# Optimization experiments

Measured on AMD Instinct MI355X. Metric: run time of the kernel, lower is better.

## Reference

```python
import jax, jax.numpy as jnp
import numpy as np

N_NODES = 100000


def _gcn_layer(x, W, b, src, dst, n):
    # PyG GCNConv with default add_self_loops=True, symmetric normalization.
    h = x @ W  # [N, out]
    deg = jax.ops.segment_sum(jnp.ones_like(dst, dtype=h.dtype), dst, num_segments=n)
    dinv = jnp.where(deg > 0, jax.lax.rsqrt(deg), 0.0)
    norm = dinv[src] * dinv[dst]  # [E]
    msg = h[src] * norm[:, None]  # gather + scale
    out = jax.ops.segment_sum(msg, dst, num_segments=n)  # scatter-add at targets
    return out + b


def setup_inputs() -> dict:
    key = jax.random.key(0)
    ks = jax.random.split(key, 8)
    n, e = N_NODES, 3200000
    x = jax.random.normal(ks[0], (n, 16), dtype=jnp.float32)
    edge_index = jax.random.randint(ks[1], (2, e), 0, n, dtype=jnp.int64)
    def glorot(k, fi, fo):
        lim = float(np.sqrt(6.0 / (fi + fo)))
        return jax.random.uniform(k, (fi, fo), jnp.float32, -lim, lim)
    return {
        "x": x,
        "edge_index": edge_index,
        "W1": glorot(ks[2], 16, 32), "b1": jnp.zeros((32,), jnp.float32),
        "W2": glorot(ks[3], 32, 64), "b2": jnp.zeros((64,), jnp.float32),
        "W3": glorot(ks[4], 64, 1),  "b3": jnp.zeros((1,), jnp.float32),
    }


def reference(x, edge_index, W1, b1, W2, b2, W3, b3):
    n = x.shape[0]
    # add self-loops once (shared by all layers)
    loops = jnp.arange(n, dtype=edge_index.dtype)
    src = jnp.concatenate([edge_index[0], loops])
    dst = jnp.concatenate([edge_index[1], loops])
    h = _gcn_layer(x, W1, b1, src, dst, n)
    h = jax.nn.relu(h)  # dropout is identity in eval mode
    h = _gcn_layer(h, W2, b2, src, dst, n)
    h = jax.nn.relu(h)
    h = _gcn_layer(h, W3, b3, src, dst, n)
    return jax.nn.sigmoid(h)
```

## Files before the change

### kernel.cpp

```cpp
#include <hip/hip_runtime.h>
#include <hip/hip_bf16.h>
#include <math.h>


#define CW    128
#define CSH   7
#define MAXBUK 1024
#define EPB   8192
#define CAP   5120

static inline int cdiv(int a, int b) { return (a + b - 1) / b; }

__device__ inline unsigned int bf16_rn(float f) {
    unsigned int u = __float_as_uint(f);
    return (u + 0x7fffu + ((u >> 16) & 1u)) >> 16;
}
#define BLO(u) __uint_as_float((u) << 16)
#define BHI(u) __uint_as_float((u) & 0xffff0000u)

#define UNPACK_ADD(A, V) \
    A[0] += BLO(V.x); A[1] += BHI(V.x); \
    A[2] += BLO(V.y); A[3] += BHI(V.y); \
    A[4] += BLO(V.z); A[5] += BHI(V.z); \
    A[6] += BLO(V.w); A[7] += BHI(V.w);
#define UNPACK_ADD2(A, V) \
    A[0] += BLO(V.x); A[1] += BHI(V.x); \
    A[2] += BLO(V.y); A[3] += BHI(V.y);


__global__ void __launch_bounds__(256) k_bscatter(const int* __restrict__ src,
                                                  const int* __restrict__ dst,
                                                  int* __restrict__ gcur,
                                                  int* __restrict__ ebuf, int e, int nbuk) {
    __shared__ int lh[MAXBUK];
    __shared__ int lo[MAXBUK];
    __shared__ int lb[MAXBUK];
    __shared__ int sh[256];
    __shared__ int stage[EPB];
    __shared__ unsigned short bkOf[EPB];
    int4 db[8];
    int t = threadIdx.x;
    for (int b = t; b < nbuk; b += 256) lh[b] = 0;
    __syncthreads();
    int base4 = blockIdx.x * (EPB / 4);
    int e4 = e >> 2;
#pragma unroll
    for (int j = 0; j < 8; j++) {
        int i4 = base4 + j * 256 + t;
        if (i4 < e4) {
            int4 d = ((const int4*)dst)[i4];
            db[j] = d;
            atomicAdd(&lh[d.x >> CSH], 1); atomicAdd(&lh[d.y >> CSH], 1);
            atomicAdd(&lh[d.z >> CSH], 1); atomicAdd(&lh[d.w >> CSH], 1);
        } else db[j] = make_int4(-1, -1, -1, -1);
    }
    __syncthreads();
    int carry = 0;
    for (int cb = 0; cb < nbuk; cb += 256) {
        int b = cb + t;
        int c = (b < nbuk) ? lh[b] : 0;
        if (b < nbuk && c) lb[b] = b * CAP + atomicAdd(&gcur[b], c);
        sh[t] = c;
        __syncthreads();
        for (int o = 1; o < 256; o <<= 1) {
            int u = (t >= o) ? sh[t - o] : 0;
            __syncthreads();
            sh[t] += u;
            __syncthreads();
        }
        if (b < nbuk) lo[b] = sh[t] - c + carry;
        carry += sh[255];
        __syncthreads();
    }
    for (int b = t; b < nbuk; b += 256) lh[b] = 0;
    __syncthreads();
#pragma unroll
    for (int j = 0; j < 8; j++) {
        int i4 = base4 + j * 256 + t;
        if (i4 < e4) {
            int4 s = ((const int4*)src)[i4];
            int4 d = db[j];
            int dd, ss, b, r, slot;
#define PUT(DX, SX) \
            dd = DX; ss = SX; b = dd >> CSH; \
            r = atomicAdd(&lh[b], 1); slot = lo[b] + r; \
            stage[slot] = ((dd & (CW - 1)) << 17) | ss; \
            bkOf[slot] = (unsigned short)b;
            PUT(d.x, s.x) PUT(d.y, s.y) PUT(d.z, s.z) PUT(d.w, s.w)
#undef PUT
        }
    }
    __syncthreads();
    int tot = min(EPB, e - blockIdx.x * EPB);
#pragma unroll
    for (int j = 0; j < 32; j++) {
        int slot = j * 256 + t;
        if (slot < tot) {
            int b = bkOf[slot];
            ebuf[lb[b] + (slot - lo[b])] = stage[slot];
        }
    }
}


__global__ void __launch_bounds__(512) k_csr2(const int* __restrict__ ebuf,
                                              const int* __restrict__ gcur,
                                              int* __restrict__ rowstart,
                                              int* __restrict__ csr_src,
                                              float* __restrict__ dinv,
                                              const float* __restrict__ x,
                                              unsigned int* __restrict__ xs,
                                              int n, int e, int nbuk) {
    __shared__ int cnt[CW];
    __shared__ int offs[CW];
    __shared__ int red[512];
    int t = threadIdx.x;
    int bid = blockIdx.x;
    int part = 0;
    for (int j = t; j < bid; j += 512) part += gcur[j];
    red[t] = part;
    __syncthreads();
    for (int o = 256; o > 0; o >>= 1) {
        if (t < o) red[t] += red[t + o];
        __syncthreads();
    }
    int dbeg = red[0];
    if (t < CW) cnt[t] = 0;
    __syncthreads();
    int cnt_b = gcur[bid];
    const int4* eb4 = (const int4*)(ebuf + (size_t)bid * CAP);
    int n4 = (cnt_b + 3) >> 2;
    for (int k4 = t; k4 < n4; k4 += 512) {
        int4 v = eb4[k4];
        int rem = cnt_b - (k4 << 2);
        atomicAdd(&cnt[v.x >> 17], 1);
        if (rem > 1) atomicAdd(&cnt[v.y >> 17], 1);
        if (rem > 2) atomicAdd(&cnt[v.z >> 17], 1);
        if (rem > 3) atomicAdd(&cnt[v.w >> 17], 1);
    }
    __syncthreads();
    int v = (t < CW) ? cnt[t] : 0;
    if (t < CW) offs[t] = v;
    __syncthreads();
    for (int o = 1; o < CW; o <<= 1) {
        int u = (t < CW && t >= o) ? offs[t - o] : 0;
        __syncthreads();
        if (t < CW) offs[t] += u;
        __syncthreads();
    }
    int node = bid * CW + t;
    if (t < CW) {
        int ex = offs[t] - v;
        float dd = rsqrtf((float)v + 1.0f);
        if (node < n) {
            rowstart[node] = dbeg + ex;
            dinv[node] = dd;
            const float4* xr = (const float4*)(x + (size_t)node * 16);
            float4 v0 = xr[0], v1 = xr[1], v2 = xr[2], v3 = xr[3];
            uint4 o0, o1;
            o0.x = bf16_rn(v0.x * dd) | (bf16_rn(v0.y * dd) << 16);
            o0.y = bf16_rn(v0.z * dd) | (bf16_rn(v0.w * dd) << 16);
            o0.z = bf16_rn(v1.x * dd) | (bf16_rn(v1.y * dd) << 16);
            o0.w = bf16_rn(v1.z * dd) | (bf16_rn(v1.w * dd) << 16);
            o1.x = bf16_rn(v2.x * dd) | (bf16_rn(v2.y * dd) << 16);
            o1.y = bf16_rn(v2.z * dd) | (bf16_rn(v2.w * dd) << 16);
            o1.z = bf16_rn(v3.x * dd) | (bf16_rn(v3.y * dd) << 16);
            o1.w = bf16_rn(v3.z * dd) | (bf16_rn(v3.w * dd) << 16);
            uint4* xo = (uint4*)(xs + (size_t)node * 8);
            xo[0] = o0; xo[1] = o1;
        }
        cnt[t] = ex;
    }
    __syncthreads();
    for (int k4 = t; k4 < n4; k4 += 512) {
        int4 vv = eb4[k4];
        int rem = cnt_b - (k4 << 2);
        int pv, r;
#define SCAT(PV) pv = PV; r = atomicAdd(&cnt[pv >> 17], 1); csr_src[dbeg + r] = pv & 0x1FFFF;
        SCAT(vv.x)
        if (rem > 1) { SCAT(vv.y) }
        if (rem > 2) { SCAT(vv.z) }
        if (rem > 3) { SCAT(vv.w) }
#undef SCAT
    }
    if (bid == 0 && t == 0) rowstart[n] = e;
}


__global__ void __launch_bounds__(256) k_pull16(const int* __restrict__ rowstart,
                                                const int* __restrict__ csr_src,
                                                const float* __restrict__ dinv,
                                                const unsigned int* __restrict__ xs,
                                                float* __restrict__ agg16, int n) {
    int wid = (blockIdx.x * blockDim.x + threadIdx.x) >> 6;
    if (wid >= n) return;
    int lane = threadIdx.x & 63;
    int q = lane & 3;
    int beg = rowstart[wid], end = rowstart[wid + 1];
    const uint2* x2 = (const uint2*)xs;
    float dd = dinv[wid];
    uint2 sv = x2[(size_t)wid * 4 + q];
    float a0[4], a1[4];
#pragma unroll
    for (int i = 0; i < 4; i++) { a0[i] = 0.f; a1[i] = 0.f; }
    int k = beg + (lane >> 2);
    for (; k + 16 < end; k += 32) {
        int s0 = __builtin_nontemporal_load(csr_src + k);
        int s1 = __builtin_nontemporal_load(csr_src + k + 16);
        uint2 v0 = x2[(size_t)s0 * 4 + q];
        uint2 v1 = x2[(size_t)s1 * 4 + q];
        UNPACK_ADD2(a0, v0);
        UNPACK_ADD2(a1, v1);
    }
    if (k < end) {
        int s0 = __builtin_nontemporal_load(csr_src + k);
        uint2 v0 = x2[(size_t)s0 * 4 + q];
        UNPACK_ADD2(a0, v0);
    }
#pragma unroll
    for (int i = 0; i < 4; i++) a0[i] += a1[i];
#pragma unroll
    for (int off = 4; off < 64; off <<= 1)
#pragma unroll
        for (int i = 0; i < 4; i++) a0[i] += __shfl_xor(a0[i], off);
    UNPACK_ADD2(a0, sv);
    if (lane < 4)
        ((float4*)(agg16 + (size_t)wid * 16))[q] =
            make_float4(a0[0] * dd, a0[1] * dd, a0[2] * dd, a0[3] * dd);
}


__global__ void __launch_bounds__(256) k_dense1(const float* __restrict__ agg,
                                                const float* __restrict__ dinv,
                                                const float* __restrict__ W1,
                                                const float* __restrict__ b1,
                                                unsigned int* __restrict__ h1s, int n) {
    int node = blockIdx.x * 256 + threadIdx.x;
    if (node >= n) return;
    float dd = dinv[node];
    float in[16];
    const float4* a4 = (const float4*)(agg + (size_t)node * 16);
#pragma unroll
    for (int f = 0; f < 4; f++) {
        float4 v = a4[f];
        in[4 * f] = v.x; in[4 * f + 1] = v.y; in[4 * f + 2] = v.z; in[4 * f + 3] = v.w;
    }
    unsigned int hw[16];
#pragma unroll
    for (int c = 0; c < 16; c++) {
        float o0 = b1[2 * c], o1 = b1[2 * c + 1];
#pragma unroll
        for (int k = 0; k < 16; k++) {
            o0 += in[k] * W1[k * 32 + 2 * c];
            o1 += in[k] * W1[k * 32 + 2 * c + 1];
        }
        hw[c] = bf16_rn(fmaxf(o0, 0.f) * dd) | (bf16_rn(fmaxf(o1, 0.f) * dd) << 16);
    }
    uint4* o4 = (uint4*)(h1s + (size_t)node * 16);
    o4[0] = make_uint4(hw[0], hw[1], hw[2], hw[3]);
    o4[1] = make_uint4(hw[4], hw[5], hw[6], hw[7]);
    o4[2] = make_uint4(hw[8], hw[9], hw[10], hw[11]);
    o4[3] = make_uint4(hw[12], hw[13], hw[14], hw[15]);
}


__global__ void __launch_bounds__(256) k_pull32(const int* __restrict__ rowstart,
                                                const int* __restrict__ csr_src,
                                                const float* __restrict__ dinv,
                                                const unsigned int* __restrict__ h1s,
                                                float* __restrict__ agg32, int n) {
    int wid = (blockIdx.x * blockDim.x + threadIdx.x) >> 6;
    if (wid >= n) return;
    int lane = threadIdx.x & 63;
    int f4 = lane & 3;
    int beg = rowstart[wid], end = rowstart[wid + 1];
    const uint4* h4 = (const uint4*)h1s;
    float dd = dinv[wid];
    uint4 sv = h4[(size_t)wid * 4 + f4];
    float acc[8], ac1[8];
#pragma unroll
    for (int i = 0; i < 8; i++) { acc[i] = 0.f; ac1[i] = 0.f; }
    int k = beg + (lane >> 2);
    for (; k + 16 < end; k += 32) {
        int s0 = __builtin_nontemporal_load(csr_src + k);
        int s1 = __builtin_nontemporal_load(csr_src + k + 16);
        uint4 v0 = h4[(size_t)s0 * 4 + f4];
        uint4 v1 = h4[(size_t)s1 * 4 + f4];
        UNPACK_ADD(acc, v0);
        UNPACK_ADD(ac1, v1);
    }
    if (k < end) {
        int s0 = __builtin_nontemporal_load(csr_src + k);
        uint4 v0 = h4[(size_t)s0 * 4 + f4];
        UNPACK_ADD(acc, v0);
    }
#pragma unroll
    for (int i = 0; i < 8; i++) acc[i] += ac1[i];
#pragma unroll
    for (int off = 4; off < 64; off <<= 1)
#pragma unroll
        for (int i = 0; i < 8; i++) acc[i] += __shfl_xor(acc[i], off);
    UNPACK_ADD(acc, sv);
    if (lane < 4) {
        float4* o4 = (float4*)(agg32 + (size_t)wid * 32 + f4 * 8);
        o4[0] = make_float4(acc[0] * dd, acc[1] * dd, acc[2] * dd, acc[3] * dd);
        o4[1] = make_float4(acc[4] * dd, acc[5] * dd, acc[6] * dd, acc[7] * dd);
    }
}


__global__ void __launch_bounds__(256) k_dense2(const float* __restrict__ agg,
                                                const float* __restrict__ dinv,
                                                const float* __restrict__ W2,
                                                const float* __restrict__ b2,
                                                const float* __restrict__ W3,
                                                float* __restrict__ t2, int n) {
    int node = blockIdx.x * 256 + threadIdx.x;
    if (node >= n) return;
    float in[32];
    const float4* a4 = (const float4*)(agg + (size_t)node * 32);
#pragma unroll
    for (int f = 0; f < 8; f++) {
        float4 v = a4[f];
        in[4 * f] = v.x; in[4 * f + 1] = v.y; in[4 * f + 2] = v.z; in[4 * f + 3] = v.w;
    }
    float p = 0.f;
#pragma unroll
    for (int cb = 0; cb < 4; cb++) {
        float o[16];
#pragma unroll
        for (int c = 0; c < 16; c++) o[c] = b2[cb * 16 + c];
#pragma unroll
        for (int k = 0; k < 32; k++) {
            float ik = in[k];
#pragma unroll
            for (int c = 0; c < 16; c++) o[c] += ik * W2[k * 64 + cb * 16 + c];
        }
#pragma unroll
        for (int c = 0; c < 16; c++) p += fmaxf(o[c], 0.f) * W3[cb * 16 + c];
    }
    t2[node] = p * dinv[node];
}


__global__ void __launch_bounds__(256) k_pull1_sig(const int* __restrict__ rowstart,
                                                   const int* __restrict__ csr_src,
                                                   const float* __restrict__ dinv,
                                                   const float* __restrict__ t2,
                                                   const float* __restrict__ b3,
                                                   float* __restrict__ out, int n) {
    int tid = blockIdx.x * blockDim.x + threadIdx.x;
    int wid = tid >> 5;
    if (wid >= n) return;
    int lane32 = threadIdx.x & 31;
    int beg = rowstart[wid], end = rowstart[wid + 1];
    float selfv = t2[wid];
    float dd = dinv[wid];
    float acc = 0.f;
    for (int k = beg + lane32; k < end; k += 32)
        acc += t2[__builtin_nontemporal_load(csr_src + k)];
#pragma unroll
    for (int off = 1; off < 32; off <<= 1) acc += __shfl_xor(acc, off);
    if (lane32 == 0) {
        float v = (acc + selfv) * dd + b3[0];
        out[wid] = 1.0f / (1.0f + expf(-v));
    }
}


extern "C" void kernel_launch(void* const* d_in, const int* in_sizes, int n_in,
                              void* d_out, int out_size, void* d_ws, size_t ws_size,
                              hipStream_t stream) {
    const float* x  = (const float*)d_in[0];
    const int*   ei = (const int*)d_in[1];
    const float* W1 = (const float*)d_in[2];
    const float* b1 = (const float*)d_in[3];
    const float* W2 = (const float*)d_in[4];
    const float* b2 = (const float*)d_in[5];
    const float* W3 = (const float*)d_in[6];
    const float* b3 = (const float*)d_in[7];

    const int n = in_sizes[0] / 16;
    const int e = in_sizes[1] / 2;
    const int* src = ei;
    const int* dst = ei + e;
    const int nbuk = cdiv(n, CW);

    auto rup = [](size_t v) { return (v + 15) & ~(size_t)15; };
    char* wp = (char*)d_ws;
    auto alloc = [&](size_t elems) { void* p = wp; wp += rup(elems) * 4; return p; };
    int*   gcur     = (int*)  alloc(MAXBUK);
    float* dinv     = (float*)alloc(n);
    int*   rowstart = (int*)  alloc(n + 1);
    int*   ebuf     = (int*)  alloc((size_t)nbuk * CAP);
    int*   csr_src  = (int*)  alloc(e);
    unsigned int* xs  = (unsigned int*)alloc((size_t)8 * n);
    unsigned int* h1s = (unsigned int*)alloc((size_t)16 * n);
    float* agg16    = (float*)alloc((size_t)16 * n);
    float* agg32    = (float*)alloc((size_t)32 * n);
    float* t2       = (float*)alloc(n);

    float* out = (float*)d_out;
    const int B = 256;
    const int pullGrid = cdiv(n * 64, B);

    hipMemsetAsync(gcur, 0, MAXBUK * 4, stream);
    k_bscatter<<<cdiv(e, EPB), B, 0, stream>>>(src, dst, gcur, ebuf, e, nbuk);
    k_csr2<<<nbuk, 512, 0, stream>>>(ebuf, gcur, rowstart, csr_src,
                                     dinv, x, xs, n, e, nbuk);

    k_pull16<<<pullGrid, B, 0, stream>>>(rowstart, csr_src, dinv, xs, agg16, n);
    k_dense1<<<cdiv(n, B), B, 0, stream>>>(agg16, dinv, W1, b1, h1s, n);

    k_pull32<<<pullGrid, B, 0, stream>>>(rowstart, csr_src, dinv, h1s, agg32, n);
    k_dense2<<<cdiv(n, B), B, 0, stream>>>(agg32, dinv, W2, b2, W3, t2, n);

    k_pull1_sig<<<cdiv(n * 32, B), B, 0, stream>>>(rowstart, csr_src, dinv, t2, b3, out, n);
}
```

Baseline: 215.7 us.

## Fuse layer-1 pull with dense transform and deepen gather unrolling

Merges the first-layer neighbor aggregation and the 16→32 dense transform into one kernel. Partial aggregates are staged in shared memory and applied to W1 by 64 threads per block, which removes the agg16 round-trip and one launch. The gather loops in the pull kernels are unrolled to three independent accumulators, and the final pull to two, to keep more loads in flight. The cost is an added block-wide barrier and a dense phase that uses only a quarter of each block's threads, with strided per-thread stores to h1s.

```diff
diff --git a/kernel.cpp b/kernel.cpp
--- a/kernel.cpp
+++ b/kernel.cpp
@@ -187,80 +187,76 @@
 }
 
 
-__global__ void __launch_bounds__(256) k_pull16(const int* __restrict__ rowstart,
-                                                const int* __restrict__ csr_src,
-                                                const float* __restrict__ dinv,
-                                                const unsigned int* __restrict__ xs,
-                                                float* __restrict__ agg16, int n) {
-    int wid = (blockIdx.x * blockDim.x + threadIdx.x) >> 6;
-    if (wid >= n) return;
-    int lane = threadIdx.x & 63;
-    int q = lane & 3;
-    int beg = rowstart[wid], end = rowstart[wid + 1];
-    const uint2* x2 = (const uint2*)xs;
-    float dd = dinv[wid];
-    uint2 sv = x2[(size_t)wid * 4 + q];
-    float a0[4], a1[4];
-#pragma unroll
-    for (int i = 0; i < 4; i++) { a0[i] = 0.f; a1[i] = 0.f; }
-    int k = beg + (lane >> 2);
-    for (; k + 16 < end; k += 32) {
-        int s0 = __builtin_nontemporal_load(csr_src + k);
-        int s1 = __builtin_nontemporal_load(csr_src + k + 16);
-        uint2 v0 = x2[(size_t)s0 * 4 + q];
-        uint2 v1 = x2[(size_t)s1 * 4 + q];
-        UNPACK_ADD2(a0, v0);
-        UNPACK_ADD2(a1, v1);
-    }
-    if (k < end) {
-        int s0 = __builtin_nontemporal_load(csr_src + k);
-        uint2 v0 = x2[(size_t)s0 * 4 + q];
-        UNPACK_ADD2(a0, v0);
-    }
-#pragma unroll
-    for (int i = 0; i < 4; i++) a0[i] += a1[i];
-#pragma unroll
-    for (int off = 4; off < 64; off <<= 1)
-#pragma unroll
-        for (int i = 0; i < 4; i++) a0[i] += __shfl_xor(a0[i], off);
-    UNPACK_ADD2(a0, sv);
-    if (lane < 4)
-        ((float4*)(agg16 + (size_t)wid * 16))[q] =
-            make_float4(a0[0] * dd, a0[1] * dd, a0[2] * dd, a0[3] * dd);
-}
-
-
-__global__ void __launch_bounds__(256) k_dense1(const float* __restrict__ agg,
-                                                const float* __restrict__ dinv,
-                                                const float* __restrict__ W1,
-                                                const float* __restrict__ b1,
-                                                unsigned int* __restrict__ h1s, int n) {
-    int node = blockIdx.x * 256 + threadIdx.x;
-    if (node >= n) return;
-    float dd = dinv[node];
-    float in[16];
-    const float4* a4 = (const float4*)(agg + (size_t)node * 16);
-#pragma unroll
-    for (int f = 0; f < 4; f++) {
-        float4 v = a4[f];
-        in[4 * f] = v.x; in[4 * f + 1] = v.y; in[4 * f + 2] = v.z; in[4 * f + 3] = v.w;
-    }
-    unsigned int hw[16];
-#pragma unroll
-    for (int c = 0; c < 16; c++) {
-        float o0 = b1[2 * c], o1 = b1[2 * c + 1];
-#pragma unroll
-        for (int k = 0; k < 16; k++) {
-            o0 += in[k] * W1[k * 32 + 2 * c];
-            o1 += in[k] * W1[k * 32 + 2 * c + 1];
-        }
-        hw[c] = bf16_rn(fmaxf(o0, 0.f) * dd) | (bf16_rn(fmaxf(o1, 0.f) * dd) << 16);
-    }
-    uint4* o4 = (uint4*)(h1s + (size_t)node * 16);
-    o4[0] = make_uint4(hw[0], hw[1], hw[2], hw[3]);
-    o4[1] = make_uint4(hw[4], hw[5], hw[6], hw[7]);
-    o4[2] = make_uint4(hw[8], hw[9], hw[10], hw[11]);
-    o4[3] = make_uint4(hw[12], hw[13], hw[14], hw[15]);
+__global__ void __launch_bounds__(256) k_pull16d(const int* __restrict__ rowstart,
+                                                 const int* __restrict__ csr_src,
+                                                 const float* __restrict__ dinv,
+                                                 const unsigned int* __restrict__ xs,
+                                                 const float* __restrict__ W1,
+                                                 const float* __restrict__ b1,
+                                                 unsigned int* __restrict__ h1s, int n) {
+    __shared__ float sAgg[4][16];
+    __shared__ float sDd[4];
+    int t = threadIdx.x;
+    int wv = t >> 6;
+    int lane = t & 63;
+    int wid = blockIdx.x * 4 + wv;
+    if (wid < n) {
+        int q = lane & 3;
+        int beg = rowstart[wid], end = rowstart[wid + 1];
+        const uint2* x2 = (const uint2*)xs;
+        float dd = dinv[wid];
+        uint2 sv = x2[(size_t)wid * 4 + q];
+        float a0[4], a1[4], a2[4];
+#pragma unroll
+        for (int i = 0; i < 4; i++) { a0[i] = 0.f; a1[i] = 0.f; a2[i] = 0.f; }
+        int k = beg + (lane >> 2);
+        for (; k + 32 < end; k += 48) {
+            int s0 = __builtin_nontemporal_load(csr_src + k);
+            int s1 = __builtin_nontemporal_load(csr_src + k + 16);
+            int s2 = __builtin_nontemporal_load(csr_src + k + 32);
+            uint2 v0 = x2[(size_t)s0 * 4 + q];
+            uint2 v1 = x2[(size_t)s1 * 4 + q];
+            uint2 v2 = x2[(size_t)s2 * 4 + q];
+            UNPACK_ADD2(a0, v0);
+            UNPACK_ADD2(a1, v1);
+            UNPACK_ADD2(a2, v2);
+        }
+        for (; k < end; k += 16) {
+            int s0 = __builtin_nontemporal_load(csr_src + k);
+            uint2 v0 = x2[(size_t)s0 * 4 + q];
+            UNPACK_ADD2(a0, v0);
+        }
+#pragma unroll
+        for (int i = 0; i < 4; i++) a0[i] += a1[i] + a2[i];
+#pragma unroll
+        for (int off = 4; off < 64; off <<= 1)
+#pragma unroll
+            for (int i = 0; i < 4; i++) a0[i] += __shfl_xor(a0[i], off);
+        UNPACK_ADD2(a0, sv);
+        if (lane < 4) {
+#pragma unroll
+            for (int i = 0; i < 4; i++) sAgg[wv][q * 4 + i] = a0[i] * dd;
+            if (q == 0) sDd[wv] = dd;
+        }
+    }
+    __syncthreads();
+    if (t < 64) {
+        int w2 = t >> 4, c = t & 15;
+        int node = blockIdx.x * 4 + w2;
+        if (node < n) {
+            float dd = sDd[w2];
+            const float* a = sAgg[w2];
+            float o0 = b1[2 * c], o1 = b1[2 * c + 1];
+#pragma unroll
+            for (int k = 0; k < 16; k++) {
+                float av = a[k];
+                o0 += av * W1[k * 32 + 2 * c];
+                o1 += av * W1[k * 32 + 2 * c + 1];
+            }
+            h1s[(size_t)node * 16 + c] =
+                bf16_rn(fmaxf(o0, 0.f) * dd) | (bf16_rn(fmaxf(o1, 0.f) * dd) << 16);
+        }
+    }
 }
 
 
@@ -277,25 +273,28 @@
     const uint4* h4 = (const uint4*)h1s;
     float dd = dinv[wid];
     uint4 sv = h4[(size_t)wid * 4 + f4];
-    float acc[8], ac1[8];
-#pragma unroll
-    for (int i = 0; i < 8; i++) { acc[i] = 0.f; ac1[i] = 0.f; }
+    float acc[8], ac1[8], ac2[8];
+#pragma unroll
+    for (int i = 0; i < 8; i++) { acc[i] = 0.f; ac1[i] = 0.f; ac2[i] = 0.f; }
     int k = beg + (lane >> 2);
-    for (; k + 16 < end; k += 32) {
+    for (; k + 32 < end; k += 48) {
         int s0 = __builtin_nontemporal_load(csr_src + k);
         int s1 = __builtin_nontemporal_load(csr_src + k + 16);
+        int s2 = __builtin_nontemporal_load(csr_src + k + 32);
         uint4 v0 = h4[(size_t)s0 * 4 + f4];
         uint4 v1 = h4[(size_t)s1 * 4 + f4];
+        uint4 v2 = h4[(size_t)s2 * 4 + f4];
         UNPACK_ADD(acc, v0);
         UNPACK_ADD(ac1, v1);
-    }
-    if (k < end) {
+        UNPACK_ADD(ac2, v2);
+    }
+    for (; k < end; k += 16) {
         int s0 = __builtin_nontemporal_load(csr_src + k);
         uint4 v0 = h4[(size_t)s0 * 4 + f4];
         UNPACK_ADD(acc, v0);
     }
 #pragma unroll
-    for (int i = 0; i < 8; i++) acc[i] += ac1[i];
+    for (int i = 0; i < 8; i++) acc[i] += ac1[i] + ac2[i];
 #pragma unroll
     for (int off = 4; off < 64; off <<= 1)
 #pragma unroll
@@ -356,9 +355,14 @@
     int beg = rowstart[wid], end = rowstart[wid + 1];
     float selfv = t2[wid];
     float dd = dinv[wid];
-    float acc = 0.f;
-    for (int k = beg + lane32; k < end; k += 32)
+    float acc = 0.f, ac1 = 0.f;
+    int k = beg + lane32;
+    for (; k + 32 < end; k += 64) {
         acc += t2[__builtin_nontemporal_load(csr_src + k)];
+        ac1 += t2[__builtin_nontemporal_load(csr_src + k + 32)];
+    }
+    if (k < end) acc += t2[__builtin_nontemporal_load(csr_src + k)];
+    acc += ac1;
 #pragma unroll
     for (int off = 1; off < 32; off <<= 1) acc += __shfl_xor(acc, off);
     if (lane32 == 0) {
@@ -396,23 +400,20 @@
     int*   csr_src  = (int*)  alloc(e);
     unsigned int* xs  = (unsigned int*)alloc((size_t)8 * n);
     unsigned int* h1s = (unsigned int*)alloc((size_t)16 * n);
-    float* agg16    = (float*)alloc((size_t)16 * n);
     float* agg32    = (float*)alloc((size_t)32 * n);
     float* t2       = (float*)alloc(n);
 
     float* out = (float*)d_out;
     const int B = 256;
-    const int pullGrid = cdiv(n * 64, B);
 
     hipMemsetAsync(gcur, 0, MAXBUK * 4, stream);
     k_bscatter<<<cdiv(e, EPB), B, 0, stream>>>(src, dst, gcur, ebuf, e, nbuk);
     k_csr2<<<nbuk, 512, 0, stream>>>(ebuf, gcur, rowstart, csr_src,
                                      dinv, x, xs, n, e, nbuk);
 
-    k_pull16<<<pullGrid, B, 0, stream>>>(rowstart, csr_src, dinv, xs, agg16, n);
-    k_dense1<<<cdiv(n, B), B, 0, stream>>>(agg16, dinv, W1, b1, h1s, n);
-
-    k_pull32<<<pullGrid, B, 0, stream>>>(rowstart, csr_src, dinv, h1s, agg32, n);
+    k_pull16d<<<cdiv(n, 4), B, 0, stream>>>(rowstart, csr_src, dinv, xs, W1, b1, h1s, n);
+
+    k_pull32<<<cdiv(n * 64, B), B, 0, stream>>>(rowstart, csr_src, dinv, h1s, agg32, n);
     k_dense2<<<cdiv(n, B), B, 0, stream>>>(agg32, dinv, W2, b2, W3, t2, n);
 
     k_pull1_sig<<<cdiv(n * 32, B), B, 0, stream>>>(rowstart, csr_src, dinv, t2, b3, out, n);
```

After: 215.6 us. About the same (-0.1%).
